# Kernel tuning notes

Hardware: AMD Instinct MI355X
Metric: run time of the kernel (lower is better)

## Reference

```python
import jax, jax.numpy as jnp
import numpy as np

B, Q, D, H, P, F = 16, 300, 256, 8, 4, 2048
HG = WG = 100          # feature-map height/width (hw = 10000, perfect square)
HW = HG * WG
DH = D // H
EPS = 1e-5


def _ln(x, g, b):
    m = x.mean(-1, keepdims=True)
    v = jnp.var(x, axis=-1, keepdims=True)
    return (x - m) * jax.lax.rsqrt(v + EPS) * g + b


def setup_inputs() -> dict:
    key = jax.random.key(0)
    ks = jax.random.split(key, 24)
    rn = lambda k, shape, s=0.02: jax.random.normal(k, shape, jnp.float32) * s
    return {
        "tgt": jax.random.normal(ks[0], (B, Q, D), jnp.float32),
        "memory": jax.random.normal(ks[1], (B, HW, D), jnp.float32),
        "in_proj_w": rn(ks[2], (D, 3 * D)), "in_proj_b": rn(ks[3], (3 * D,)),
        "out_proj_w": rn(ks[4], (D, D)), "out_proj_b": rn(ks[5], (D,)),
        "norm1_g": jnp.ones((D,), jnp.float32), "norm1_b": jnp.zeros((D,), jnp.float32),
        "ref_w": rn(ks[6], (D, 2)), "ref_b": rn(ks[7], (2,)),
        "off_w": rn(ks[8], (D, H * P * 2)), "off_b": rn(ks[9], (H * P * 2,)),
        "attw_w": rn(ks[10], (D, H * P)), "attw_b": rn(ks[11], (H * P,)),
        "vproj_w": rn(ks[12], (D, D)), "vproj_b": rn(ks[13], (D,)),
        "oproj_w": rn(ks[14], (D, D)), "oproj_b": rn(ks[15], (D,)),
        "norm2_g": jnp.ones((D,), jnp.float32), "norm2_b": jnp.zeros((D,), jnp.float32),
        "lin1_w": rn(ks[16], (D, F)), "lin1_b": rn(ks[17], (F,)),
        "lin2_w": rn(ks[18], (F, D)), "lin2_b": rn(ks[19], (D,)),
        "norm3_g": jnp.ones((D,), jnp.float32), "norm3_b": jnp.zeros((D,), jnp.float32),
    }


def reference(tgt, memory, in_proj_w, in_proj_b, out_proj_w, out_proj_b,
              norm1_g, norm1_b, ref_w, ref_b, off_w, off_b, attw_w, attw_b,
              vproj_w, vproj_b, oproj_w, oproj_b, norm2_g, norm2_b,
              lin1_w, lin1_b, lin2_w, lin2_b, norm3_g, norm3_b):
    # ---- self-attention (nn.MultiheadAttention, eval mode: dropout = identity)
    qkv = tgt @ in_proj_w + in_proj_b                      # [B,Q,3D]
    q, k, v = jnp.split(qkv, 3, axis=-1)
    q = q.reshape(B, Q, H, DH)
    k = k.reshape(B, Q, H, DH)
    v = v.reshape(B, Q, H, DH)
    scores = jnp.einsum('bqhd,bkhd->bhqk', q, k) / jnp.sqrt(jnp.float32(DH))
    attn = jax.nn.softmax(scores, axis=-1)
    sa = jnp.einsum('bhqk,bkhd->bqhd', attn, v).reshape(B, Q, D) @ out_proj_w + out_proj_b
    x = _ln(tgt + sa, norm1_g, norm1_b)

    # ---- reference points
    ref = jax.nn.sigmoid(x @ ref_w + ref_b)                # [B,Q,2] in (0,1)

    # ---- deformable cross-attention
    offs = (x @ off_w + off_b).reshape(B, Q, H, P, 2)
    wts = jax.nn.softmax((x @ attw_w + attw_b).reshape(B, Q, H, P), axis=-1)
    vals = (memory @ vproj_w + vproj_b).reshape(B, HW, H, DH)
    loc = jnp.clip(ref[:, :, None, None, :] + offs, 0.0, 1.0)
    sx = loc[..., 0] * (WG - 1)
    sy = loc[..., 1] * (HG - 1)
    x0 = jnp.floor(sx)
    y0 = jnp.floor(sy)
    x0i = jnp.clip(x0.astype(jnp.int32), 0, WG - 1)
    y0i = jnp.clip(y0.astype(jnp.int32), 0, HG - 1)
    x1i = jnp.clip(x0i + 1, 0, WG - 1)
    y1i = jnp.clip(y0i + 1, 0, HG - 1)
    wx1 = sx - x0
    wx0 = 1.0 - wx1
    wy1 = sy - y0
    wy0 = 1.0 - wy1
    bi = jnp.arange(B)[:, None, None, None]
    hi = jnp.arange(H)[None, None, :, None]

    def gather(yi, xi):                                    # [B,Q,H,P,DH]
        return vals[bi, yi * WG + xi, hi]

    samp = (gather(y0i, x0i) * (wx0 * wy0)[..., None]
            + gather(y1i, x0i) * (wx0 * wy1)[..., None]
            + gather(y0i, x1i) * (wx1 * wy0)[..., None]
            + gather(y1i, x1i) * (wx1 * wy1)[..., None])
    ca = (samp * wts[..., None]).sum(axis=3).reshape(B, Q, D) @ oproj_w + oproj_b
    x = _ln(x + ca, norm2_g, norm2_b)

    # ---- FFN
    ff = jax.nn.relu(x @ lin1_w + lin1_b) @ lin2_w + lin2_b
    return _ln(x + ff, norm3_g, norm3_b)
```

## Files before the change

### kernel.cpp

```cpp
#include <hip/hip_runtime.h>

#define NB   16
#define NQ   300
#define ND   256
#define NH   8
#define NP   4
#define NF   2048
#define NHW  10000
#define NWG  100
#define NROW 4800

typedef __attribute__((ext_vector_type(8))) short bf16x8;
typedef __attribute__((ext_vector_type(4))) float f32x4;

__device__ __forceinline__ unsigned short f2bf(float f) {
    unsigned u = __builtin_bit_cast(unsigned, f);
    u = (u + 0x7fffu + ((u >> 16) & 1u)) >> 16;
    return (unsigned short)u;
}
__device__ __forceinline__ float bf2f(unsigned short h) {
    unsigned u = ((unsigned)h) << 16;
    return __builtin_bit_cast(float, u);
}

__global__ __launch_bounds__(256) void transpose_cast(
    const float* __restrict__ w_in,  const float* __restrict__ w_out,
    const float* __restrict__ w_vp,  const float* __restrict__ w_op,
    const float* __restrict__ w_l1,  const float* __restrict__ w_l2,
    unsigned short* __restrict__ o_in, unsigned short* __restrict__ o_out,
    unsigned short* __restrict__ o_vp, unsigned short* __restrict__ o_op,
    unsigned short* __restrict__ o_l1, unsigned short* __restrict__ o_l2)
{
    __shared__ float ts[64][65];
    int b = blockIdx.x;
    const float* src; unsigned short* dst; int K, N, ncx;
    if      (b < 48)  { src = w_in;  dst = o_in;  K = 256;  N = 768;  ncx = 12; }
    else if (b < 64)  { src = w_out; dst = o_out; K = 256;  N = 256;  ncx = 4;  b -= 48; }
    else if (b < 80)  { src = w_vp;  dst = o_vp;  K = 256;  N = 256;  ncx = 4;  b -= 64; }
    else if (b < 96)  { src = w_op;  dst = o_op;  K = 256;  N = 256;  ncx = 4;  b -= 80; }
    else if (b < 224) { src = w_l1;  dst = o_l1;  K = 256;  N = 2048; ncx = 32; b -= 96; }
    else              { src = w_l2;  dst = o_l2;  K = 2048; N = 256;  ncx = 4;  b -= 224; }
    const int n0 = (b % ncx) * 64, k0 = (b / ncx) * 64;
    const int t = threadIdx.x;
    const int r = t >> 4, c = t & 15;
    #pragma unroll
    for (int j = 0; j < 4; j++) {
        float4 v = *(const float4*)(src + (long)(k0 + j * 16 + r) * N + n0 + c * 4);
        ts[j * 16 + r][c * 4 + 0] = v.x;
        ts[j * 16 + r][c * 4 + 1] = v.y;
        ts[j * 16 + r][c * 4 + 2] = v.z;
        ts[j * 16 + r][c * 4 + 3] = v.w;
    }
    __syncthreads();
    #pragma unroll
    for (int j = 0; j < 4; j++) {
        unsigned short o[4];
        #pragma unroll
        for (int i = 0; i < 4; i++)
            o[i] = f2bf(ts[c * 4 + i][j * 16 + r]);
        *(uint2*)(dst + (long)(n0 + j * 16 + r) * K + k0 + c * 4) = *(uint2*)o;
    }
}

__global__ __launch_bounds__(256) void prep_head(
    const float* __restrict__ rw, const float* __restrict__ rb,
    const float* __restrict__ ow, const float* __restrict__ ob,
    const float* __restrict__ aw, const float* __restrict__ ab,
    unsigned short* __restrict__ o_hd, float* __restrict__ o_hb)
{
    int id = blockIdx.x * 256 + threadIdx.x;
    if (id < 32768) {
        int n = id >> 8, k = id & 255;
        float v;
        if (n < 2)       v = rw[k * 2 + n];
        else if (n < 66) v = ow[k * 64 + (n - 2)];
        else if (n < 98) v = aw[k * 32 + (n - 66)];
        else             v = 0.0f;
        o_hd[id] = f2bf(v);
        return;
    }
    id -= 32768;
    if (id < 128) {
        float v;
        if (id < 2)       v = rb[id];
        else if (id < 66) v = ob[id - 2];
        else if (id < 98) v = ab[id - 66];
        else              v = 0.0f;
        o_hb[id] = v;
    }
}

__global__ __launch_bounds__(256, 2) void gemm_vproj(
    const float* __restrict__ A, const unsigned short* __restrict__ Bt,
    const float* __restrict__ bias, unsigned short* __restrict__ Cout)
{
    __shared__ unsigned short As[2][128][40];
    __shared__ unsigned short Bs[2][256][40];
    const int t    = threadIdx.x;
    const long m0  = (long)blockIdx.x * 128;
    const int  wave = t >> 6, lane = t & 63;
    const int  wm  = (wave >> 1) << 6;
    const int  wn  = (wave & 1) << 7;
    const int  l16 = lane & 15, quad = lane >> 4;
    const int  arow = t >> 3, acol = (t & 7) << 2;
    const int  brow = t >> 2, bcol = (t & 3) << 3;

    f32x4 acc[4][8] = {};
    float4 fa[4];
    uint4  fb[4];

    auto loadAB = [&](int k0) {
        #pragma unroll
        for (int j = 0; j < 4; j++)
            fa[j] = *(const float4*)(A + (m0 + j * 32 + arow) * 256L + k0 + acol);
        #pragma unroll
        for (int j = 0; j < 4; j++)
            fb[j] = *(const uint4*)(Bt + (j * 64 + brow) * 256L + k0 + bcol);
    };
    auto storeLDS = [&](int buf) {
        #pragma unroll
        for (int j = 0; j < 4; j++) {
            unsigned short ta[4] = {f2bf(fa[j].x), f2bf(fa[j].y),
                                    f2bf(fa[j].z), f2bf(fa[j].w)};
            *(uint2*)&As[buf][j * 32 + arow][acol] = *(uint2*)ta;
        }
        #pragma unroll
        for (int j = 0; j < 4; j++)
            *(uint4*)&Bs[buf][j * 64 + brow][bcol] = fb[j];
    };

    loadAB(0);
    storeLDS(0);
    __syncthreads();

    for (int kt = 0; kt < 8; kt++) {
        const int cur = kt & 1;
        if (kt < 7) loadAB((kt + 1) * 32);

        bf16x8 af[4], bfr[8];
        #pragma unroll
        for (int i = 0; i < 4; i++)
            af[i] = *(const bf16x8*)&As[cur][wm + i * 16 + l16][quad * 8];
        #pragma unroll
        for (int j = 0; j < 8; j++)
            bfr[j] = *(const bf16x8*)&Bs[cur][wn + j * 16 + l16][quad * 8];
        #pragma unroll
        for (int i = 0; i < 4; i++)
            #pragma unroll
            for (int j = 0; j < 8; j++)
                acc[i][j] = __builtin_amdgcn_mfma_f32_16x16x32_bf16(
                    bfr[j], af[i], acc[i][j], 0, 0, 0);

        if (kt < 7) {
            storeLDS(cur ^ 1);
            __syncthreads();
        }
    }

    float4 bj[8];
    #pragma unroll
    for (int j = 0; j < 8; j++)
        bj[j] = *(const float4*)&bias[wn + j * 16 + quad * 4];

    #pragma unroll
    for (int i = 0; i < 4; i++) {
        const long gr = m0 + wm + i * 16 + l16;
        #pragma unroll
        for (int j = 0; j < 8; j++) {
            const int gc = wn + j * 16 + quad * 4;
            unsigned short o[4] = {f2bf(acc[i][j][0] + bj[j].x),
                                   f2bf(acc[i][j][1] + bj[j].y),
                                   f2bf(acc[i][j][2] + bj[j].z),
                                   f2bf(acc[i][j][3] + bj[j].w)};
            *(uint2*)(Cout + gr * 256 + gc) = *(uint2*)o;
        }
    }
}

template <int RELU, int OUTBF, int SPLITK, int TM>
__global__ __launch_bounds__(256, (TM == 64) ? 4 : 3) void gemm_bt(
    const float* __restrict__ A, const unsigned short* __restrict__ Bt,
    const float* __restrict__ bias, void* __restrict__ Cout,
    int M, int N, int K)
{
    constexpr int AI = TM / 32;
    constexpr int NI = TM / 32;
    __shared__ unsigned short As[2][TM][40];
    __shared__ unsigned short Bs[2][128][40];
    const int t    = threadIdx.x;
    const long m0  = (long)blockIdx.y * TM;
    const int  n0  = blockIdx.x * 128;
    const int  wave = t >> 6, lane = t & 63;
    const int  wm  = (wave >> 1) * (TM / 2);
    const int  wn  = (wave & 1) << 6;
    const int  l16 = lane & 15, quad = lane >> 4;
    const int  arow = t >> 3, acol = (t & 7) << 2;
    const int  brow = t >> 2, bcol = (t & 3) << 3;

    f32x4 acc[NI][4] = {};

    const int kChunk = K / SPLITK;
    const int kBeg   = (SPLITK > 1) ? blockIdx.z * kChunk : 0;
    const int nk     = kChunk / 32;

    float4 fa[AI];
    uint4  fb[2];

    auto loadAB = [&](int kt) {
        const int k0 = kBeg + kt * 32;
        #pragma unroll
        for (int j = 0; j < AI; j++) {
            const long r = m0 + j * 32 + arow;
            fa[j] = (r < M) ? *(const float4*)(A + r * (long)K + k0 + acol)
                            : make_float4(0.f, 0.f, 0.f, 0.f);
        }
        #pragma unroll
        for (int j = 0; j < 2; j++)
            fb[j] = *(const uint4*)(Bt + (long)(n0 + j * 64 + brow) * K + k0 + bcol);
    };
    auto storeLDS = [&](int buf) {
        #pragma unroll
        for (int j = 0; j < AI; j++) {
            unsigned short ta[4] = {f2bf(fa[j].x), f2bf(fa[j].y),
                                    f2bf(fa[j].z), f2bf(fa[j].w)};
            *(uint2*)&As[buf][j * 32 + arow][acol] = *(uint2*)ta;
        }
        #pragma unroll
        for (int j = 0; j < 2; j++)
            *(uint4*)&Bs[buf][j * 64 + brow][bcol] = fb[j];
    };

    loadAB(0);
    storeLDS(0);
    __syncthreads();

    for (int kt = 0; kt < nk; kt++) {
        const int cur = kt & 1;
        if (kt + 1 < nk) loadAB(kt + 1);

        bf16x8 af[NI], bfr[4];
        #pragma unroll
        for (int i = 0; i < NI; i++)
            af[i] = *(const bf16x8*)&As[cur][wm + i * 16 + l16][quad * 8];
        #pragma unroll
        for (int j = 0; j < 4; j++)
            bfr[j] = *(const bf16x8*)&Bs[cur][wn + j * 16 + l16][quad * 8];
        #pragma unroll
        for (int i = 0; i < NI; i++)
            #pragma unroll
            for (int j = 0; j < 4; j++)
                acc[i][j] = __builtin_amdgcn_mfma_f32_16x16x32_bf16(
                    bfr[j], af[i], acc[i][j], 0, 0, 0);

        if (kt + 1 < nk) {
            storeLDS(cur ^ 1);
            __syncthreads();
        }
    }

    float4 bj[4];
    #pragma unroll
    for (int j = 0; j < 4; j++)
        bj[j] = *(const float4*)&bias[n0 + wn + j * 16 + quad * 4];

    float* outp = (float*)Cout;
    float bscale = 1.0f;
    if (SPLITK > 1) {
        outp += (size_t)blockIdx.z * M * N;
        bscale = (blockIdx.z == 0) ? 1.0f : 0.0f;
    }

    #pragma unroll
    for (int i = 0; i < NI; i++) {
        const long gr = m0 + wm + i * 16 + l16;
        if (gr < M) {
            #pragma unroll
            for (int j = 0; j < 4; j++) {
                float4 v;
                v.x = acc[i][j][0] + bscale * bj[j].x;
                v.y = acc[i][j][1] + bscale * bj[j].y;
                v.z = acc[i][j][2] + bscale * bj[j].z;
                v.w = acc[i][j][3] + bscale * bj[j].w;
                if (RELU) {
                    v.x = fmaxf(v.x, 0.f); v.y = fmaxf(v.y, 0.f);
                    v.z = fmaxf(v.z, 0.f); v.w = fmaxf(v.w, 0.f);
                }
                const int gc = n0 + wn + j * 16 + quad * 4;
                if (OUTBF) {
                    unsigned short o[4] = {f2bf(v.x), f2bf(v.y), f2bf(v.z), f2bf(v.w)};
                    *(uint2*)((unsigned short*)Cout + gr * N + gc) = *(uint2*)o;
                } else {
                    *(float4*)(outp + gr * N + gc) = v;
                }
            }
        }
    }
}

__global__ __launch_bounds__(256) void attn_kernel(
    const float* __restrict__ qkv, float* __restrict__ sa)
{
    __shared__ union {
        struct {
            unsigned short Ks[304][40];
            unsigned short Qs[64][40];
        } s;
        unsigned short Ps[4][16][328];
    } u;
    __shared__ unsigned short Vt[32][328];

    const int bh = blockIdx.y;
    const int b  = bh >> 3, h = bh & 7;
    const int q0 = blockIdx.x * 64;
    const int t  = threadIdx.x;

    for (int idx = t; idx < 304 * 8; idx += 256) {
        const int r = idx >> 3, c4 = (idx & 7) << 2;
        if (r < NQ) {
            const float4 kv = *(const float4*)(qkv + ((long)(b * NQ + r)) * 768 + 256 + h * 32 + c4);
            u.s.Ks[r][c4 + 0] = f2bf(kv.x); u.s.Ks[r][c4 + 1] = f2bf(kv.y);
            u.s.Ks[r][c4 + 2] = f2bf(kv.z); u.s.Ks[r][c4 + 3] = f2bf(kv.w);
        } else {
            u.s.Ks[r][c4 + 0] = 0; u.s.Ks[r][c4 + 1] = 0;
            u.s.Ks[r][c4 + 2] = 0; u.s.Ks[r][c4 + 3] = 0;
        }
    }
    for (int idx = t; idx < NQ * 8; idx += 256) {
        const int key = idx >> 3, dq = (idx & 7) << 2;
        const float4 vv = *(const float4*)(qkv + ((long)(b * NQ + key)) * 768 + 512 + h * 32 + dq);
        Vt[dq + 0][key] = f2bf(vv.x); Vt[dq + 1][key] = f2bf(vv.y);
        Vt[dq + 2][key] = f2bf(vv.z); Vt[dq + 3][key] = f2bf(vv.w);
    }
    for (int idx = t; idx < 32 * 20; idx += 256)
        Vt[idx / 20][300 + idx % 20] = 0;
    for (int idx = t; idx < 64 * 8; idx += 256) {
        const int r = idx >> 3, c4 = (idx & 7) << 2;
        const int q = q0 + r;
        if (q < NQ) {
            const float4 qv = *(const float4*)(qkv + ((long)(b * NQ + q)) * 768 + h * 32 + c4);
            u.s.Qs[r][c4 + 0] = f2bf(qv.x); u.s.Qs[r][c4 + 1] = f2bf(qv.y);
            u.s.Qs[r][c4 + 2] = f2bf(qv.z); u.s.Qs[r][c4 + 3] = f2bf(qv.w);
        } else {
            u.s.Qs[r][c4 + 0] = 0; u.s.Qs[r][c4 + 1] = 0;
            u.s.Qs[r][c4 + 2] = 0; u.s.Qs[r][c4 + 3] = 0;
        }
    }
    __syncthreads();

    const int wave = t >> 6, lane = t & 63;
    const int l16 = lane & 15, quad = lane >> 4;
    const float scale = 0.1767766952966369f;

    const bf16x8 aq = *(const bf16x8*)&u.s.Qs[wave * 16 + l16][quad * 8];
    f32x4 sacc[19];
    #pragma unroll
    for (int kt = 0; kt < 19; kt++) {
        const bf16x8 bk = *(const bf16x8*)&u.s.Ks[kt * 16 + l16][quad * 8];
        sacc[kt] = __builtin_amdgcn_mfma_f32_16x16x32_bf16(
            aq, bk, (f32x4){0.f, 0.f, 0.f, 0.f}, 0, 0, 0);
    }

    float inv[4];
    #pragma unroll
    for (int r = 0; r < 4; r++) {
        float m = -1e30f;
        #pragma unroll
        for (int kt = 0; kt < 19; kt++) {
            float s = sacc[kt][r] * scale;
            if (kt == 18 && l16 >= 12) s = -1e30f;
            sacc[kt][r] = s;
            m = fmaxf(m, s);
        }
        m = fmaxf(m, __shfl_xor(m, 1)); m = fmaxf(m, __shfl_xor(m, 2));
        m = fmaxf(m, __shfl_xor(m, 4)); m = fmaxf(m, __shfl_xor(m, 8));
        float sum = 0.f;
        #pragma unroll
        for (int kt = 0; kt < 19; kt++) {
            float p = __expf(sacc[kt][r] - m);
            sacc[kt][r] = p;
            sum += p;
        }
        sum += __shfl_xor(sum, 1); sum += __shfl_xor(sum, 2);
        sum += __shfl_xor(sum, 4); sum += __shfl_xor(sum, 8);
        inv[r] = 1.0f / sum;
    }

    __syncthreads();

    #pragma unroll
    for (int kt = 0; kt < 19; kt++)
        #pragma unroll
        for (int r = 0; r < 4; r++)
            u.Ps[wave][quad * 4 + r][kt * 16 + l16] = f2bf(sacc[kt][r] * inv[r]);
    #pragma unroll
    for (int r = 0; r < 4; r++)
        u.Ps[wave][quad * 4 + r][304 + l16] = 0;

    f32x4 o0 = {0.f, 0.f, 0.f, 0.f}, o1 = {0.f, 0.f, 0.f, 0.f};
    #pragma unroll
    for (int kt = 0; kt < 10; kt++) {
        const bf16x8 ap  = *(const bf16x8*)&u.Ps[wave][l16][kt * 32 + quad * 8];
        const bf16x8 bv0 = *(const bf16x8*)&Vt[l16][kt * 32 + quad * 8];
        const bf16x8 bv1 = *(const bf16x8*)&Vt[16 + l16][kt * 32 + quad * 8];
        o0 = __builtin_amdgcn_mfma_f32_16x16x32_bf16(ap, bv0, o0, 0, 0, 0);
        o1 = __builtin_amdgcn_mfma_f32_16x16x32_bf16(ap, bv1, o1, 0, 0, 0);
    }

    #pragma unroll
    for (int r = 0; r < 4; r++) {
        const int q = q0 + wave * 16 + quad * 4 + r;
        if (q < NQ) {
            float* op = sa + ((long)(b * NQ + q)) * ND + h * 32;
            op[l16]      = o0[r];
            op[16 + l16] = o1[r];
        }
    }
}

template <int NPART>
__global__ __launch_bounds__(256) void residual_ln(
    const float* __restrict__ a, const float* __restrict__ r,
    const float* __restrict__ gam, const float* __restrict__ bet,
    float* __restrict__ out, long pstride)
{
    const int row  = blockIdx.x * 4 + (threadIdx.x >> 6);
    const int lane = threadIdx.x & 63;
    const long base = (long)row * ND + lane * 4;
    float4 av = *(const float4*)(a + base);
    float4 rv = *(const float4*)(r + base);
    #pragma unroll
    for (int z = 1; z < NPART; z++) {
        float4 pv = *(const float4*)(r + z * pstride + base);
        rv.x += pv.x; rv.y += pv.y; rv.z += pv.z; rv.w += pv.w;
    }
    float x0 = av.x + rv.x, x1 = av.y + rv.y, x2 = av.z + rv.z, x3 = av.w + rv.w;
    float s  = x0 + x1 + x2 + x3;
    float s2 = x0 * x0 + x1 * x1 + x2 * x2 + x3 * x3;
    #pragma unroll
    for (int off = 32; off >= 1; off >>= 1) {
        s  += __shfl_xor(s, off);
        s2 += __shfl_xor(s2, off);
    }
    float mean = s * 0.00390625f;
    float var  = s2 * 0.00390625f - mean * mean;
    float rstd = rsqrtf(var + 1e-5f);
    float4 gv = *(const float4*)(gam + lane * 4);
    float4 bv = *(const float4*)(bet + lane * 4);
    float4 o;
    o.x = (x0 - mean) * rstd * gv.x + bv.x;
    o.y = (x1 - mean) * rstd * gv.y + bv.y;
    o.z = (x2 - mean) * rstd * gv.z + bv.z;
    o.w = (x3 - mean) * rstd * gv.w + bv.w;
    *(float4*)(out + base) = o;
}

__global__ __launch_bounds__(256) void meta_kernel(
    const float* __restrict__ res, float* __restrict__ meta)
{
    const int t   = threadIdx.x;
    const int row = blockIdx.x * 8 + (t >> 5);
    const int s   = t & 31;
    const int h   = s >> 2;
    const float* rp = res + (long)row * 128;
    const float rx = 1.f / (1.f + __expf(-rp[0]));
    const float ry = 1.f / (1.f + __expf(-rp[1]));
    const float offx = rp[2 + 2 * s], offy = rp[3 + 2 * s];
    const float a0 = rp[66 + h * 4 + 0], a1 = rp[66 + h * 4 + 1];
    const float a2 = rp[66 + h * 4 + 2], a3 = rp[66 + h * 4 + 3];
    const float mx = fmaxf(fmaxf(a0, a1), fmaxf(a2, a3));
    const float den = __expf(a0 - mx) + __expf(a1 - mx) +
                      __expf(a2 - mx) + __expf(a3 - mx);
    const float awt = __expf(rp[66 + s] - mx) / den;

    const float lx = fminf(fmaxf(rx + offx, 0.f), 1.f) * (NWG - 1);
    const float ly = fminf(fmaxf(ry + offy, 0.f), 1.f) * (NWG - 1);
    const float fx = floorf(lx), fy = floorf(ly);
    int x0 = (int)fx; x0 = min(max(x0, 0), NWG - 1);
    int y0 = (int)fy; y0 = min(max(y0, 0), NWG - 1);
    const int x1 = min(x0 + 1, NWG - 1);
    const int y1 = min(y0 + 1, NWG - 1);
    const float wx1 = lx - fx, wx0 = 1.f - wx1;
    const float wy1 = ly - fy, wy0 = 1.f - wy1;
    float4 m0, m1;
    m0.x = __int_as_float(y0 * NWG + x0);
    m0.y = __int_as_float(y0 * NWG + x1);
    m0.z = __int_as_float(y1 * NWG + x0);
    m0.w = __int_as_float(y1 * NWG + x1);
    m1.x = awt * wx0 * wy0;
    m1.y = awt * wx1 * wy0;
    m1.z = awt * wx0 * wy1;
    m1.w = awt * wx1 * wy1;
    float* mp = meta + (long)row * 256 + s * 8;
    *(float4*)mp       = m0;
    *(float4*)(mp + 4) = m1;
}

__global__ __launch_bounds__(256) void deform_gather(
    const float* __restrict__ meta, const unsigned short* __restrict__ vals,
    float* __restrict__ ca)
{
    const int row = blockIdx.x;
    const int b = row / NQ;
    __shared__ float ms[256];
    const int t = threadIdx.x;
    ms[t] = meta[(long)row * 256 + t];
    __syncthreads();
    const int h = t >> 5, d = t & 31;
    const unsigned short* vb = vals + (long)b * NHW * ND + h * 32 + d;
    float acc = 0.f;
    #pragma unroll
    for (int p = 0; p < NP; p++) {
        const float* mp = ms + h * 32 + p * 8;
        const int i00 = __float_as_int(mp[0]);
        const int i01 = __float_as_int(mp[1]);
        const int i10 = __float_as_int(mp[2]);
        const int i11 = __float_as_int(mp[3]);
        acc += mp[4] * bf2f(vb[(long)i00 * ND]);
        acc += mp[5] * bf2f(vb[(long)i01 * ND]);
        acc += mp[6] * bf2f(vb[(long)i10 * ND]);
        acc += mp[7] * bf2f(vb[(long)i11 * ND]);
    }
    ca[(long)row * ND + t] = acc;
}

extern "C" void kernel_launch(void* const* d_in, const int* in_sizes, int n_in,
                              void* d_out, int out_size, void* d_ws, size_t ws_size,
                              hipStream_t stream)
{
    (void)in_sizes; (void)n_in; (void)out_size; (void)ws_size;
    const float* tgt   = (const float*)d_in[0];
    const float* mem   = (const float*)d_in[1];
    const float* inpw  = (const float*)d_in[2];
    const float* inpb  = (const float*)d_in[3];
    const float* outw  = (const float*)d_in[4];
    const float* outb  = (const float*)d_in[5];
    const float* n1g   = (const float*)d_in[6];
    const float* n1b   = (const float*)d_in[7];
    const float* refw  = (const float*)d_in[8];
    const float* refb  = (const float*)d_in[9];
    const float* offw  = (const float*)d_in[10];
    const float* offb  = (const float*)d_in[11];
    const float* attww = (const float*)d_in[12];
    const float* attwb = (const float*)d_in[13];
    const float* vpw   = (const float*)d_in[14];
    const float* vpb   = (const float*)d_in[15];
    const float* opw   = (const float*)d_in[16];
    const float* opb   = (const float*)d_in[17];
    const float* n2g   = (const float*)d_in[18];
    const float* n2b   = (const float*)d_in[19];
    const float* l1w   = (const float*)d_in[20];
    const float* l1b   = (const float*)d_in[21];
    const float* l2w   = (const float*)d_in[22];
    const float* l2b   = (const float*)d_in[23];
    const float* n3g   = (const float*)d_in[24];
    const float* n3b   = (const float*)d_in[25];
    float* out = (float*)d_out;

    char* p = (char*)d_ws;
    auto alloc = [&](size_t bytes) {
        char* r = p; p += (bytes + 255) & ~(size_t)255; return (void*)r;
    };
    unsigned short* wtIn   = (unsigned short*)alloc(768 * 256 * 2);
    unsigned short* wtOut  = (unsigned short*)alloc(256 * 256 * 2);
    unsigned short* wtVp   = (unsigned short*)alloc(256 * 256 * 2);
    unsigned short* wtOp   = (unsigned short*)alloc(256 * 256 * 2);
    unsigned short* wtL1   = (unsigned short*)alloc(2048 * 256 * 2);
    unsigned short* wtL2   = (unsigned short*)alloc(256 * 2048 * 2);
    unsigned short* wtHead = (unsigned short*)alloc(128 * 256 * 2);
    float*          headb  = (float*)alloc(128 * 4);
    float* qkv  = (float*)alloc((size_t)NROW * 768 * 4);
    float* sa   = (float*)alloc((size_t)NROW * ND * 4);
    float* x1   = (float*)alloc((size_t)NROW * ND * 4);
    float* x2   = (float*)alloc((size_t)NROW * ND * 4);
    float* tmp  = (float*)alloc((size_t)NROW * ND * 4 * 4);
    float* ca   = (float*)alloc((size_t)NROW * ND * 4);
    float* meta = (float*)alloc((size_t)NROW * 256 * 4);
    void* uni = alloc((size_t)NB * NHW * ND * 2);
    unsigned short* vals = (unsigned short*)uni;
    float* h1 = (float*)uni;
    float* res = qkv;

    transpose_cast<<<352, 256, 0, stream>>>(
        inpw, outw, vpw, opw, l1w, l2w,
        wtIn, wtOut, wtVp, wtOp, wtL1, wtL2);
    prep_head<<<129, 256, 0, stream>>>(refw, refb, offw, offb, attww, attwb,
                                       wtHead, headb);

    gemm_bt<0, 0, 1, 64><<<dim3(6, 75), 256, 0, stream>>>(tgt, wtIn, inpb, qkv,
                                                          NROW, 768, 256);
    gemm_vproj<<<1250, 256, 0, stream>>>(mem, wtVp, vpb, vals);
    attn_kernel<<<dim3(5, 128), 256, 0, stream>>>(qkv, sa);
    gemm_bt<0, 0, 1, 64><<<dim3(2, 75), 256, 0, stream>>>(sa, wtOut, outb, tmp,
                                                          NROW, 256, 256);
    residual_ln<1><<<1200, 256, 0, stream>>>(tgt, tmp, n1g, n1b, x1, 0);
    gemm_bt<0, 0, 1, 64><<<dim3(1, 75), 256, 0, stream>>>(x1, wtHead, headb, res,
                                                          NROW, 128, 256);
    meta_kernel<<<600, 256, 0, stream>>>(res, meta);
    deform_gather<<<4800, 256, 0, stream>>>(meta, vals, ca);
    gemm_bt<0, 0, 1, 64><<<dim3(2, 75), 256, 0, stream>>>(ca, wtOp, opb, tmp,
                                                          NROW, 256, 256);
    residual_ln<1><<<1200, 256, 0, stream>>>(x1, tmp, n2g, n2b, x2, 0);
    gemm_bt<1, 0, 1, 64><<<dim3(16, 75), 256, 0, stream>>>(x2, wtL1, l1b, h1,
                                                           NROW, 2048, 256);
    gemm_bt<0, 0, 4, 64><<<dim3(2, 75, 4), 256, 0, stream>>>(h1, wtL2, l2b, tmp,
                                                             NROW, 256, 2048);
    residual_ln<4><<<1200, 256, 0, stream>>>(x2, tmp, n3g, n3b, out,
                                             (long)NROW * ND);
}
```

Measured before the change: 520.7 us.

## Load GEMM B tiles via direct global-to-LDS and unify vproj into gemm_bt

```diff
diff --git a/kernel.cpp b/kernel.cpp
--- a/kernel.cpp
+++ b/kernel.cpp
@@ -21,6 +21,13 @@
 __device__ __forceinline__ float bf2f(unsigned short h) {
     unsigned u = ((unsigned)h) << 16;
     return __builtin_bit_cast(float, u);
+}
+
+__device__ __forceinline__ void gl_lds16(const unsigned short* g, unsigned short* l) {
+    __builtin_amdgcn_global_load_lds(
+        (__attribute__((address_space(1))) const void*)g,
+        (__attribute__((address_space(3))) void*)l,
+        16, 0, 0);
 }
 
 __global__ __launch_bounds__(256) void transpose_cast(
@@ -90,170 +97,76 @@
     }
 }
 
-__global__ __launch_bounds__(256, 2) void gemm_vproj(
-    const float* __restrict__ A, const unsigned short* __restrict__ Bt,
-    const float* __restrict__ bias, unsigned short* __restrict__ Cout)
-{
-    __shared__ unsigned short As[2][128][40];
-    __shared__ unsigned short Bs[2][256][40];
-    const int t    = threadIdx.x;
-    const long m0  = (long)blockIdx.x * 128;
-    const int  wave = t >> 6, lane = t & 63;
-    const int  wm  = (wave >> 1) << 6;
-    const int  wn  = (wave & 1) << 7;
-    const int  l16 = lane & 15, quad = lane >> 4;
-    const int  arow = t >> 3, acol = (t & 7) << 2;
-    const int  brow = t >> 2, bcol = (t & 3) << 3;
-
-    f32x4 acc[4][8] = {};
-    float4 fa[4];
-    uint4  fb[4];
-
-    auto loadAB = [&](int k0) {
-        #pragma unroll
-        for (int j = 0; j < 4; j++)
-            fa[j] = *(const float4*)(A + (m0 + j * 32 + arow) * 256L + k0 + acol);
-        #pragma unroll
-        for (int j = 0; j < 4; j++)
-            fb[j] = *(const uint4*)(Bt + (j * 64 + brow) * 256L + k0 + bcol);
-    };
-    auto storeLDS = [&](int buf) {
-        #pragma unroll
-        for (int j = 0; j < 4; j++) {
-            unsigned short ta[4] = {f2bf(fa[j].x), f2bf(fa[j].y),
-                                    f2bf(fa[j].z), f2bf(fa[j].w)};
-            *(uint2*)&As[buf][j * 32 + arow][acol] = *(uint2*)ta;
-        }
-        #pragma unroll
-        for (int j = 0; j < 4; j++)
-            *(uint4*)&Bs[buf][j * 64 + brow][bcol] = fb[j];
-    };
-
-    loadAB(0);
-    storeLDS(0);
-    __syncthreads();
-
-    for (int kt = 0; kt < 8; kt++) {
-        const int cur = kt & 1;
-        if (kt < 7) loadAB((kt + 1) * 32);
-
-        bf16x8 af[4], bfr[8];
-        #pragma unroll
-        for (int i = 0; i < 4; i++)
-            af[i] = *(const bf16x8*)&As[cur][wm + i * 16 + l16][quad * 8];
-        #pragma unroll
-        for (int j = 0; j < 8; j++)
-            bfr[j] = *(const bf16x8*)&Bs[cur][wn + j * 16 + l16][quad * 8];
-        #pragma unroll
-        for (int i = 0; i < 4; i++)
-            #pragma unroll
-            for (int j = 0; j < 8; j++)
-                acc[i][j] = __builtin_amdgcn_mfma_f32_16x16x32_bf16(
-                    bfr[j], af[i], acc[i][j], 0, 0, 0);
-
-        if (kt < 7) {
-            storeLDS(cur ^ 1);
-            __syncthreads();
-        }
-    }
-
-    float4 bj[8];
-    #pragma unroll
-    for (int j = 0; j < 8; j++)
-        bj[j] = *(const float4*)&bias[wn + j * 16 + quad * 4];
-
-    #pragma unroll
-    for (int i = 0; i < 4; i++) {
-        const long gr = m0 + wm + i * 16 + l16;
-        #pragma unroll
-        for (int j = 0; j < 8; j++) {
-            const int gc = wn + j * 16 + quad * 4;
-            unsigned short o[4] = {f2bf(acc[i][j][0] + bj[j].x),
-                                   f2bf(acc[i][j][1] + bj[j].y),
-                                   f2bf(acc[i][j][2] + bj[j].z),
-                                   f2bf(acc[i][j][3] + bj[j].w)};
-            *(uint2*)(Cout + gr * 256 + gc) = *(uint2*)o;
-        }
-    }
-}
-
 template <int RELU, int OUTBF, int SPLITK, int TM>
-__global__ __launch_bounds__(256, (TM == 64) ? 4 : 3) void gemm_bt(
+__global__ __launch_bounds__(256, 4) void gemm_bt(
     const float* __restrict__ A, const unsigned short* __restrict__ Bt,
     const float* __restrict__ bias, void* __restrict__ Cout,
     int M, int N, int K)
 {
-    constexpr int AI = TM / 32;
-    constexpr int NI = TM / 32;
-    __shared__ unsigned short As[2][TM][40];
-    __shared__ unsigned short Bs[2][128][40];
+    static_assert(TM == 64, "tile is 64x128");
+    __shared__ __align__(16) unsigned short As[2][64 * 32];
+    __shared__ __align__(16) unsigned short Bs[2][128 * 32];
     const int t    = threadIdx.x;
-    const long m0  = (long)blockIdx.y * TM;
+    const long m0  = (long)blockIdx.y * 64;
     const int  n0  = blockIdx.x * 128;
     const int  wave = t >> 6, lane = t & 63;
-    const int  wm  = (wave >> 1) * (TM / 2);
+    const int  l16 = lane & 15, quad = lane >> 4;
+    const int  wm  = (wave >> 1) << 5;
     const int  wn  = (wave & 1) << 6;
-    const int  l16 = lane & 15, quad = lane >> 4;
-    const int  arow = t >> 3, acol = (t & 7) << 2;
-    const int  brow = t >> 2, bcol = (t & 3) << 3;
-
-    f32x4 acc[NI][4] = {};
+    const int  fA  = (wave >> 1) << 1;
+    const int  fB  = (wave & 1) << 2;
+
+    f32x4 acc[2][4] = {};
 
     const int kChunk = K / SPLITK;
     const int kBeg   = (SPLITK > 1) ? blockIdx.z * kChunk : 0;
     const int nk     = kChunk / 32;
 
-    float4 fa[AI];
-    uint4  fb[2];
-
-    auto loadAB = [&](int kt) {
-        const int k0 = kBeg + kt * 32;
-        #pragma unroll
-        for (int j = 0; j < AI; j++) {
-            const long r = m0 + j * 32 + arow;
-            fa[j] = (r < M) ? *(const float4*)(A + r * (long)K + k0 + acol)
-                            : make_float4(0.f, 0.f, 0.f, 0.f);
-        }
-        #pragma unroll
-        for (int j = 0; j < 2; j++)
-            fb[j] = *(const uint4*)(Bt + (long)(n0 + j * 64 + brow) * K + k0 + bcol);
+    const float* aP =
+        A + (m0 + wave * 16 + l16) * (long)K + kBeg + (quad << 3);
+    const unsigned short* bP =
+        Bt + (long)(n0 + wave * 32 + l16) * K + kBeg + (quad << 3);
+    unsigned short* aW  = &As[0][(wave << 9) + (lane << 3)];
+    unsigned short* bW0 = &Bs[0][(wave << 10)];
+
+    float4 fa0, fa1;
+    auto loadA = [&](int kt) {
+        fa0 = *(const float4*)(aP + kt * 32);
+        fa1 = *(const float4*)(aP + kt * 32 + 4);
     };
-    auto storeLDS = [&](int buf) {
-        #pragma unroll
-        for (int j = 0; j < AI; j++) {
-            unsigned short ta[4] = {f2bf(fa[j].x), f2bf(fa[j].y),
-                                    f2bf(fa[j].z), f2bf(fa[j].w)};
-            *(uint2*)&As[buf][j * 32 + arow][acol] = *(uint2*)ta;
-        }
-        #pragma unroll
-        for (int j = 0; j < 2; j++)
-            *(uint4*)&Bs[buf][j * 64 + brow][bcol] = fb[j];
+    auto issueB = [&](int kt, int buf) {
+        gl_lds16(bP + kt * 32,          bW0 + buf * 4096);
+        gl_lds16(bP + kt * 32 + 16 * K, bW0 + buf * 4096 + 512);
     };
-
-    loadAB(0);
-    storeLDS(0);
+    auto writeA = [&](int buf) {
+        unsigned short ta[8] = {f2bf(fa0.x), f2bf(fa0.y), f2bf(fa0.z), f2bf(fa0.w),
+                                f2bf(fa1.x), f2bf(fa1.y), f2bf(fa1.z), f2bf(fa1.w)};
+        *(uint4*)(aW + buf * 2048) = *(const uint4*)ta;
+    };
+
+    loadA(0);
+    issueB(0, 0);
+    writeA(0);
     __syncthreads();
 
     for (int kt = 0; kt < nk; kt++) {
         const int cur = kt & 1;
-        if (kt + 1 < nk) loadAB(kt + 1);
-
-        bf16x8 af[NI], bfr[4];
+        if (kt + 1 < nk) {
+            issueB(kt + 1, cur ^ 1);
+            loadA(kt + 1);
+        }
+
+        const bf16x8 af0 = *(const bf16x8*)&As[cur][(fA + 0) * 512 + (lane << 3)];
+        const bf16x8 af1 = *(const bf16x8*)&As[cur][(fA + 1) * 512 + (lane << 3)];
         #pragma unroll
-        for (int i = 0; i < NI; i++)
-            af[i] = *(const bf16x8*)&As[cur][wm + i * 16 + l16][quad * 8];
-        #pragma unroll
-        for (int j = 0; j < 4; j++)
-            bfr[j] = *(const bf16x8*)&Bs[cur][wn + j * 16 + l16][quad * 8];
-        #pragma unroll
-        for (int i = 0; i < NI; i++)
-            #pragma unroll
-            for (int j = 0; j < 4; j++)
-                acc[i][j] = __builtin_amdgcn_mfma_f32_16x16x32_bf16(
-                    bfr[j], af[i], acc[i][j], 0, 0, 0);
+        for (int j = 0; j < 4; j++) {
+            const bf16x8 bv = *(const bf16x8*)&Bs[cur][(fB + j) * 512 + (lane << 3)];
+            acc[0][j] = __builtin_amdgcn_mfma_f32_16x16x32_bf16(bv, af0, acc[0][j], 0, 0, 0);
+            acc[1][j] = __builtin_amdgcn_mfma_f32_16x16x32_bf16(bv, af1, acc[1][j], 0, 0, 0);
+        }
 
         if (kt + 1 < nk) {
-            storeLDS(cur ^ 1);
+            writeA(cur ^ 1);
             __syncthreads();
         }
     }
@@ -261,7 +174,7 @@
     float4 bj[4];
     #pragma unroll
     for (int j = 0; j < 4; j++)
-        bj[j] = *(const float4*)&bias[n0 + wn + j * 16 + quad * 4];
+        bj[j] = *(const float4*)&bias[n0 + wn + j * 16 + (quad << 2)];
 
     float* outp = (float*)Cout;
     float bscale = 1.0f;
@@ -271,27 +184,25 @@
     }
 
     #pragma unroll
-    for (int i = 0; i < NI; i++) {
+    for (int i = 0; i < 2; i++) {
         const long gr = m0 + wm + i * 16 + l16;
-        if (gr < M) {
-            #pragma unroll
-            for (int j = 0; j < 4; j++) {
-                float4 v;
-                v.x = acc[i][j][0] + bscale * bj[j].x;
-                v.y = acc[i][j][1] + bscale * bj[j].y;
-                v.z = acc[i][j][2] + bscale * bj[j].z;
-                v.w = acc[i][j][3] + bscale * bj[j].w;
-                if (RELU) {
-                    v.x = fmaxf(v.x, 0.f); v.y = fmaxf(v.y, 0.f);
-                    v.z = fmaxf(v.z, 0.f); v.w = fmaxf(v.w, 0.f);
-                }
-                const int gc = n0 + wn + j * 16 + quad * 4;
-                if (OUTBF) {
-                    unsigned short o[4] = {f2bf(v.x), f2bf(v.y), f2bf(v.z), f2bf(v.w)};
-                    *(uint2*)((unsigned short*)Cout + gr * N + gc) = *(uint2*)o;
-                } else {
-                    *(float4*)(outp + gr * N + gc) = v;
-                }
+        #pragma unroll
+        for (int j = 0; j < 4; j++) {
+            float4 v;
+            v.x = acc[i][j][0] + bscale * bj[j].x;
+            v.y = acc[i][j][1] + bscale * bj[j].y;
+            v.z = acc[i][j][2] + bscale * bj[j].z;
+            v.w = acc[i][j][3] + bscale * bj[j].w;
+            if (RELU) {
+                v.x = fmaxf(v.x, 0.f); v.y = fmaxf(v.y, 0.f);
+                v.z = fmaxf(v.z, 0.f); v.w = fmaxf(v.w, 0.f);
+            }
+            const int gc = n0 + wn + j * 16 + (quad << 2);
+            if (OUTBF) {
+                unsigned short o[4] = {f2bf(v.x), f2bf(v.y), f2bf(v.z), f2bf(v.w)};
+                *(uint2*)((unsigned short*)Cout + gr * N + gc) = *(uint2*)o;
+            } else {
+                *(float4*)(outp + gr * N + gc) = v;
             }
         }
     }
@@ -588,7 +499,8 @@
 
     gemm_bt<0, 0, 1, 64><<<dim3(6, 75), 256, 0, stream>>>(tgt, wtIn, inpb, qkv,
                                                           NROW, 768, 256);
-    gemm_vproj<<<1250, 256, 0, stream>>>(mem, wtVp, vpb, vals);
+    gemm_bt<0, 1, 1, 64><<<dim3(2, 2500), 256, 0, stream>>>(mem, wtVp, vpb, vals,
+                                                            NB * NHW, 256, 256);
     attn_kernel<<<dim3(5, 128), 256, 0, stream>>>(qkv, sa);
     gemm_bt<0, 0, 1, 64><<<dim3(2, 75), 256, 0, stream>>>(sa, wtOut, outb, tmp,
                                                           NROW, 256, 256);
@@ -605,5 +517,5 @@
     gemm_bt<0, 0, 4, 64><<<dim3(2, 75, 4), 256, 0, stream>>>(h1, wtL2, l2b, tmp,
                                                              NROW, 256, 2048);
     residual_ln<4><<<1200, 256, 0, stream>>>(x2, tmp, n3g, n3b, out,
-                                             (long)NROW * ND);
-}
+                                             (long)NROW * 256);
+}
```

Result: no change. 514.9 us (-1.1%).
